# Kernel optimization log

Hardware: AMD Instinct MI355X
Metric: run time of the kernel (lower is better)

The kernel has to match this reference:

```python
import jax, jax.numpy as jnp
import numpy as np

EPS = 1e-5

def _ln(x, g, b):
    mu = jnp.mean(x, axis=-1, keepdims=True)
    var = jnp.mean(jnp.square(x - mu), axis=-1, keepdims=True)
    return (x - mu) * jax.lax.rsqrt(var + EPS) * g + b

def setup_inputs() -> dict:
    key = jax.random.key(0)
    ks = jax.random.split(key, 16)
    B, L, D, H = 1, 512, 128, 128  # d_pair=128, d_hidden=128
    s_d = 1.0 / np.sqrt(D)
    s_h = 1.0 / np.sqrt(H)
    return {
        "pair": jax.random.normal(ks[0], (B, L, L, D), jnp.float32),
        "ln_g": jnp.ones((D,), jnp.float32),
        "ln_b": jnp.zeros((D,), jnp.float32),
        "lw": jax.random.normal(ks[1], (H, D), jnp.float32) * s_d,
        "lb": jnp.zeros((H,), jnp.float32),
        "lgw": jax.random.normal(ks[2], (H, D), jnp.float32) * s_d,
        "lgb": jnp.ones((H,), jnp.float32),
        "rw": jax.random.normal(ks[3], (H, D), jnp.float32) * s_d,
        "rb": jnp.zeros((H,), jnp.float32),
        "rgw": jax.random.normal(ks[4], (H, D), jnp.float32) * s_d,
        "rgb": jnp.ones((H,), jnp.float32),
        "gw": jax.random.normal(ks[5], (D, D), jnp.float32) * s_d,
        "gb": jnp.ones((D,), jnp.float32),
        "lno_g": jnp.ones((H,), jnp.float32),
        "lno_b": jnp.zeros((H,), jnp.float32),
        "ow": jax.random.normal(ks[6], (D, H), jnp.float32) * s_h,
        "ob": jnp.zeros((D,), jnp.float32),
    }

def reference(pair, ln_g, ln_b, lw, lb, lgw, lgb, rw, rb, rgw, rgb, gw, gb, lno_g, lno_b, ow, ob):
    L = pair.shape[1]
    p = _ln(pair, ln_g, ln_b)                                   # [B,L,L,D]
    left = jax.nn.sigmoid(p @ lgw.T + lgb) * (p @ lw.T + lb)    # [B,L,L,H]
    right = jax.nn.sigmoid(p @ rgw.T + rgb) * (p @ rw.T + rb)   # [B,L,L,H]
    # outgoing: contract over k (second seq dim)
    out = jnp.einsum('bikd,bjkd->bijd', left, right / jnp.float32(L))
    out = _ln(out, lno_g, lno_b)
    out = out @ ow.T + ob                                       # [B,L,L,D]
    gate = jax.nn.sigmoid(p @ gw.T + gb)
    return gate * out
```

## Files before the change

### kernel.cpp

```cpp
#include <hip/hip_runtime.h>
#include <hip/hip_bf16.h>
#include <stdint.h>

#define LSEQ 512
#define LL   262144

typedef __attribute__((ext_vector_type(8))) short short8;
typedef __attribute__((ext_vector_type(4))) float f32x4;
typedef __attribute__((ext_vector_type(4))) unsigned short us4;
typedef __attribute__((ext_vector_type(8))) unsigned short us8;

static_assert(sizeof(short8) == 16, "");
static_assert(sizeof(us8) == 16, "");

__device__ inline unsigned short f2bf(float f){
  unsigned u = __builtin_bit_cast(unsigned, f);
  unsigned r = (u + 0x7fffu + ((u >> 16) & 1u)) >> 16;
  return (unsigned short)r;
}
__device__ inline float bf2f(unsigned short s){
  return __builtin_bit_cast(float, ((unsigned)s) << 16);
}
__device__ inline float sigm(float x){ return 1.f / (1.f + __expf(-x)); }

__device__ inline int sw256(int row, int byte_in_row){
  return row*256 + ((((byte_in_row >> 4) ^ (row & 7))) << 4) + (byte_in_row & 15);
}
__device__ inline int sw128(int row, int byte_in_row){
  return row*128 + ((((byte_in_row >> 4) ^ (row & 7))) << 4) + (byte_in_row & 15);
}

__device__ inline void gload16(const void* g, void* lds){
  __builtin_amdgcn_global_load_lds(
      (const __attribute__((address_space(1))) unsigned*)g,
      (__attribute__((address_space(3))) unsigned*)lds, 16, 0, 0);
}

__global__ __launch_bounds__(128) void k0_prep(
    const float* __restrict__ ow, const float* __restrict__ lnog,
    const float* __restrict__ lnob, const float* __restrict__ ob,
    unsigned short* __restrict__ wgbf, float* __restrict__ swg, float* __restrict__ swb)
{
  const int dd = blockIdx.x;
  const int t  = threadIdx.x;
  const int idx = dd*128 + t;
  float o = ow[idx];
  float a = o * lnog[t];
  float b = o * lnob[t];
  wgbf[idx] = f2bf(a);
  #pragma unroll
  for (int m = 1; m < 64; m <<= 1){ a += __shfl_xor(a, m); b += __shfl_xor(b, m); }
  __shared__ float sA[2], sB[2];
  if ((t & 63) == 0){ sA[t >> 6] = a; sB[t >> 6] = b; }
  __syncthreads();
  if (t == 0){ swg[dd] = sA[0] + sA[1]; swb[dd] = sB[0] + sB[1] + ob[dd]; }
}

__global__ __launch_bounds__(64) void kP_pack(
    const float* __restrict__ lgw, const float* __restrict__ lw,
    const float* __restrict__ rgw, const float* __restrict__ rw,
    const float* __restrict__ gw, short8* __restrict__ wpk)
{
  const int b = blockIdx.x;
  const int arm = b >> 5, n = (b >> 2) & 7, ks = b & 3;
  const float* src = arm==0 ? lgw : arm==1 ? lw : arm==2 ? rgw : arm==3 ? rw : gw;
  const int l = threadIdx.x;
  const int h = n*16 + (l & 15), k0 = ks*32 + (l >> 4)*8;
  short8 v;
  #pragma unroll
  for (int e = 0; e < 8; ++e) v[e] = (short)f2bf(src[h*128 + k0 + e]);
  wpk[b*64 + l] = v;
}

__global__ __launch_bounds__(256, 4) void k1_proj(
    const float* __restrict__ pair, const float* __restrict__ ln_g, const float* __restrict__ ln_b,
    const float* __restrict__ lb,  const float* __restrict__ lgb,
    const float* __restrict__ rb,  const float* __restrict__ rgb,
    const float* __restrict__ gb,
    const short8* __restrict__ wpk,
    unsigned short* __restrict__ lt, unsigned short* __restrict__ rt,
    unsigned short* __restrict__ gate)
{
  __shared__ char p_l[16384];
  const int t = threadIdx.x;
  const int w = t >> 6, l = t & 63;
  const long pos0 = (long)blockIdx.x * 64;

  {
    const int q8 = t & 7;
    float4 g4[4], b4[4];
    #pragma unroll
    for (int i = 0; i < 4; ++i){
      g4[i] = *(const float4*)(ln_g + q8*4 + i*32);
      b4[i] = *(const float4*)(ln_b + q8*4 + i*32);
    }
    #pragma unroll
    for (int pass = 0; pass < 2; ++pass){
      const int row = pass*32 + (t >> 3);
      float4 x[4];
      #pragma unroll
      for (int i = 0; i < 4; ++i)
        x[i] = *(const float4*)(pair + (pos0 + row)*128 + q8*4 + i*32);
      float s = 0.f, qq = 0.f;
      #pragma unroll
      for (int i = 0; i < 4; ++i){
        s  += (x[i].x + x[i].y) + (x[i].z + x[i].w);
        qq += (x[i].x*x[i].x + x[i].y*x[i].y) + (x[i].z*x[i].z + x[i].w*x[i].w);
      }
      #pragma unroll
      for (int msk = 1; msk < 8; msk <<= 1){ s += __shfl_xor(s, msk); qq += __shfl_xor(qq, msk); }
      const float mu = s * (1.f/128.f);
      const float rs = rsqrtf(qq * (1.f/128.f) - mu*mu + 1e-5f);
      #pragma unroll
      for (int i = 0; i < 4; ++i){
        us4 o;
        o.x = f2bf((x[i].x - mu)*rs*g4[i].x + b4[i].x);
        o.y = f2bf((x[i].y - mu)*rs*g4[i].y + b4[i].y);
        o.z = f2bf((x[i].z - mu)*rs*g4[i].z + b4[i].z);
        o.w = f2bf((x[i].w - mu)*rs*g4[i].w + b4[i].w);
        *(us4*)(p_l + sw256(row, q8*8 + i*64)) = o;
      }
    }
  }
  __syncthreads();

  f32x4 aG[4][2], aL[4][2];
  auto zero = [&](f32x4 (&acc)[4][2]){
    #pragma unroll
    for (int m = 0; m < 4; ++m){ acc[m][0] = f32x4{0,0,0,0}; acc[m][1] = f32x4{0,0,0,0}; }
  };
  auto gemm2 = [&](int armG, int armL){
    #pragma unroll
    for (int ks = 0; ks < 4; ++ks){
      short8 av[4];
      #pragma unroll
      for (int m = 0; m < 4; ++m)
        av[m] = *(const short8*)(p_l + sw256(m*16 + (l & 15), ks*64 + (l >> 4)*16));
      #pragma unroll
      for (int n2 = 0; n2 < 2; ++n2){
        const int n = w*2 + n2;
        const short8 bg = wpk[((armG*8 + n)*4 + ks)*64 + l];
        const short8 bl = wpk[((armL*8 + n)*4 + ks)*64 + l];
        #pragma unroll
        for (int m = 0; m < 4; ++m){
          aG[m][n2] = __builtin_amdgcn_mfma_f32_16x16x32_bf16(av[m], bg, aG[m][n2], 0, 0, 0);
          aL[m][n2] = __builtin_amdgcn_mfma_f32_16x16x32_bf16(av[m], bl, aL[m][n2], 0, 0, 0);
        }
      }
    }
  };
  auto epiDirect = [&](const float* __restrict__ gbias, const float* __restrict__ lbias,
                       unsigned short* __restrict__ dst){
    #pragma unroll
    for (int n2 = 0; n2 < 2; ++n2){
      const int h = w*32 + n2*16 + (l & 15);
      const float gv = gbias[h], lv = lbias[h];
      #pragma unroll
      for (int m = 0; m < 4; ++m){
        us4 o;
        #pragma unroll
        for (int r = 0; r < 4; ++r)
          o[r] = f2bf(sigm(aG[m][n2][r] + gv) * (aL[m][n2][r] + lv));
        *(us4*)(dst + (long)h*LL + pos0 + m*16 + (l >> 4)*4) = o;
      }
    }
  };

  zero(aG); zero(aL); gemm2(0, 1); epiDirect(lgb, lb, lt);
  zero(aG); zero(aL); gemm2(2, 3); epiDirect(rgb, rb, rt);

  zero(aG);
  #pragma unroll
  for (int ks = 0; ks < 4; ++ks){
    short8 av[4];
    #pragma unroll
    for (int m = 0; m < 4; ++m)
      av[m] = *(const short8*)(p_l + sw256(m*16 + (l & 15), ks*64 + (l >> 4)*16));
    #pragma unroll
    for (int n2 = 0; n2 < 2; ++n2){
      const int n = w*2 + n2;
      const short8 bg = wpk[((4*8 + n)*4 + ks)*64 + l];
      #pragma unroll
      for (int m = 0; m < 4; ++m)
        aG[m][n2] = __builtin_amdgcn_mfma_f32_16x16x32_bf16(av[m], bg, aG[m][n2], 0, 0, 0);
    }
  }
  __syncthreads();
  #pragma unroll
  for (int n2 = 0; n2 < 2; ++n2){
    const int h = w*32 + n2*16 + (l & 15);
    const float gv = gb[h];
    #pragma unroll
    for (int m = 0; m < 4; ++m)
      #pragma unroll
      for (int r = 0; r < 4; ++r){
        const int pos = m*16 + (l >> 4)*4 + r;
        *(unsigned short*)(p_l + sw256(pos, h*2)) = f2bf(sigm(aG[m][n2][r] + gv));
      }
  }
  __syncthreads();
  #pragma unroll
  for (int p = 0; p < 4; ++p){
    const int row = p*16 + (t >> 4), ch = t & 15;
    us8 v = *(const us8*)(p_l + sw256(row, ch*16));
    *(us8*)(gate + (pos0 + row)*128 + ch*8) = v;
  }
}

__global__ __launch_bounds__(256) void k2_tri(
    const unsigned short* __restrict__ lt, const unsigned short* __restrict__ rt,
    unsigned short* __restrict__ omm)
{
  __shared__ char smem[32768];
  char* As = smem;
  char* Bs = smem + 16384;
  const int t = threadIdx.x;
  const int b0 = blockIdx.x;
  const int b  = (b0 & 7) * 256 + (b0 >> 3);
  const int d = b >> 4, tile = b & 15;
  const int i0 = (tile >> 2)*128, j0 = (tile & 3)*128;
  const unsigned short* Ag = lt + (long)d*LL;
  const unsigned short* Bg = rt + (long)d*LL;
  const int w = t >> 6, l = t & 63;
  const int wm = w >> 1, wn = w & 1;

  f32x4 acc[4][4];
  #pragma unroll
  for (int m = 0; m < 4; ++m)
    #pragma unroll
    for (int n = 0; n < 4; ++n) acc[m][n] = f32x4{0.f,0.f,0.f,0.f};

  for (int kt = 0; kt < 8; ++kt){
    const int k0 = kt*64;
    __syncthreads();
    #pragma unroll
    for (int q = 0; q < 4; ++q){
      int P = q*4096 + t*16;
      int row = P >> 7;
      int ls  = ((P >> 4) & 7) ^ (row & 7);
      gload16(Ag + (long)(i0 + row)*512 + k0 + ls*8, As + P);
      gload16(Bg + (long)(j0 + row)*512 + k0 + ls*8, Bs + P);
    }
    __syncthreads();
    #pragma unroll
    for (int ks = 0; ks < 2; ++ks){
      short8 a[4], bb[4];
      #pragma unroll
      for (int m = 0; m < 4; ++m){
        int row = wm*64 + m*16 + (l & 15);
        a[m] = *(const short8*)(As + sw128(row, ks*64 + (l >> 4)*16));
      }
      #pragma unroll
      for (int n = 0; n < 4; ++n){
        int row = wn*64 + n*16 + (l & 15);
        bb[n] = *(const short8*)(Bs + sw128(row, ks*64 + (l >> 4)*16));
      }
      #pragma unroll
      for (int m = 0; m < 4; ++m)
        #pragma unroll
        for (int n = 0; n < 4; ++n)
          acc[m][n] = __builtin_amdgcn_mfma_f32_16x16x32_bf16(a[m], bb[n], acc[m][n], 0, 0, 0);
    }
  }
  __syncthreads();
  #pragma unroll
  for (int m = 0; m < 4; ++m)
    #pragma unroll
    for (int n = 0; n < 4; ++n)
      #pragma unroll
      for (int r = 0; r < 4; ++r){
        int row = wm*64 + m*16 + (l >> 4)*4 + r;
        int j   = wn*64 + n*16 + (l & 15);
        *(unsigned short*)(smem + sw256(row, j*2)) = f2bf(acc[m][n][r] * (1.f/512.f));
      }
  __syncthreads();
  #pragma unroll
  for (int it = 0; it < 8; ++it){
    int row = it*16 + (t >> 4), ch = t & 15;
    us8 v = *(const us8*)(smem + sw256(row, ch*16));
    *(us8*)(omm + (long)d*LL + (long)(i0 + row)*512 + j0 + ch*8) = v;
  }
}

__global__ __launch_bounds__(256) void k3_out(
    const unsigned short* __restrict__ omm, const unsigned short* __restrict__ gate,
    const unsigned short* __restrict__ wgbf,
    const float* __restrict__ swg, const float* __restrict__ swb,
    float* __restrict__ out)
{
  __shared__ char omm_l[32768];
  __shared__ char wg_l[32768];
  __shared__ float mu_s[128], rs_s[128];
  const int t = threadIdx.x;
  const int jt = blockIdx.x, i = blockIdx.y;
  const int j0 = jt*128;
  const int w = t >> 6, l = t & 63;

  {
    const int jc = t & 15, dg = t >> 4;
    float sum[8], sq[8];
    #pragma unroll
    for (int e = 0; e < 8; ++e){ sum[e] = 0.f; sq[e] = 0.f; }
    #pragma unroll
    for (int q = 0; q < 8; ++q){
      int dd = dg + q*16;
      us8 v = *(const us8*)(omm + (long)dd*LL + (long)i*512 + j0 + jc*8);
      *(us8*)(omm_l + dd*256 + jc*16) = v;
      #pragma unroll
      for (int e = 0; e < 8; ++e){
        float f = bf2f(v[e]);
        sum[e] += f; sq[e] += f*f;
      }
    }
    float* scr = (float*)wg_l;
    #pragma unroll
    for (int e = 0; e < 8; ++e){
      scr[dg*128 + jc*8 + e]        = sum[e];
      scr[2048 + dg*128 + jc*8 + e] = sq[e];
    }
  }
  __syncthreads();
  if (t < 128){
    const float* scr = (const float*)wg_l;
    float s1 = 0.f, s2 = 0.f;
    #pragma unroll
    for (int g = 0; g < 16; ++g){ s1 += scr[g*128 + t]; s2 += scr[2048 + g*128 + t]; }
    float mu = s1 * (1.f/128.f);
    float var = s2 * (1.f/128.f) - mu*mu;
    mu_s[t] = mu;
    rs_s[t] = rsqrtf(var + 1e-5f);
  }
  __syncthreads();
  #pragma unroll
  for (int q = 0; q < 8; ++q){
    int P = q*4096 + t*16;
    gload16((const char*)wgbf + sw256(P >> 8, P & 255), wg_l + P);
  }
  __syncthreads();

  f32x4 acc[2][8];
  #pragma unroll
  for (int m = 0; m < 2; ++m)
    #pragma unroll
    for (int n = 0; n < 8; ++n) acc[m][n] = f32x4{0.f,0.f,0.f,0.f};

  #pragma unroll
  for (int ks = 0; ks < 4; ++ks){
    short8 a[2];
    #pragma unroll
    for (int m = 0; m < 2; ++m){
      const int jj = w*32 + m*16 + (l & 15);
      short8 av;
      #pragma unroll
      for (int e = 0; e < 8; ++e){
        int dd = ks*32 + (l >> 4)*8 + e;
        av[e] = *(const short*)(omm_l + dd*256 + jj*2);
      }
      a[m] = av;
    }
    #pragma unroll
    for (int n = 0; n < 8; ++n){
      int row = n*16 + (l & 15);
      short8 bb = *(const short8*)(wg_l + sw256(row, ks*64 + (l >> 4)*16));
      #pragma unroll
      for (int m = 0; m < 2; ++m)
        acc[m][n] = __builtin_amdgcn_mfma_f32_16x16x32_bf16(a[m], bb, acc[m][n], 0, 0, 0);
    }
  }

  float swgv[8], swbv[8];
  #pragma unroll
  for (int n = 0; n < 8; ++n){ swgv[n] = swg[n*16 + (l & 15)]; swbv[n] = swb[n*16 + (l & 15)]; }
  #pragma unroll
  for (int m = 0; m < 2; ++m){
    #pragma unroll
    for (int r = 0; r < 4; ++r){
      int j = w*32 + m*16 + (l >> 4)*4 + r;
      float mu = mu_s[j], rs = rs_s[j];
      long rowoff = ((long)i*512 + j0 + j)*128;
      #pragma unroll
      for (int n = 0; n < 8; ++n){
        int ddx = n*16 + (l & 15);
        float val = rs*(acc[m][n][r] - mu*swgv[n]) + swbv[n];
        out[rowoff + ddx] = val * bf2f(gate[rowoff + ddx]);
      }
    }
  }
}

extern "C" void kernel_launch(void* const* d_in, const int* in_sizes, int n_in,
                              void* d_out, int out_size, void* d_ws, size_t ws_size,
                              hipStream_t stream)
{
  const float* pair = (const float*)d_in[0];
  const float* ln_g = (const float*)d_in[1];
  const float* ln_b = (const float*)d_in[2];
  const float* lw   = (const float*)d_in[3];
  const float* lb   = (const float*)d_in[4];
  const float* lgw  = (const float*)d_in[5];
  const float* lgb  = (const float*)d_in[6];
  const float* rw   = (const float*)d_in[7];
  const float* rb   = (const float*)d_in[8];
  const float* rgw  = (const float*)d_in[9];
  const float* rgb  = (const float*)d_in[10];
  const float* gw   = (const float*)d_in[11];
  const float* gb   = (const float*)d_in[12];
  const float* lnog = (const float*)d_in[13];
  const float* lnob = (const float*)d_in[14];
  const float* ow   = (const float*)d_in[15];
  const float* ob   = (const float*)d_in[16];
  float* out = (float*)d_out;

  char* ws = (char*)d_ws;
  unsigned short* lt   = (unsigned short*)(ws);
  unsigned short* rt   = (unsigned short*)(ws + (1l << 26));
  unsigned short* gate = (unsigned short*)(ws + (2l << 26));
  unsigned short* omm  = (unsigned short*)(ws + (3l << 26));
  short8*         wpk  = (short8*)(ws + (3l << 26));
  unsigned short* wgbf = (unsigned short*)(ws + (4l << 26));
  float* swg = (float*)(ws + (4l << 26) + 65536);
  float* swb = swg + 128;

  k0_prep<<<dim3(128), dim3(128), 0, stream>>>(ow, lnog, lnob, ob, wgbf, swg, swb);
  kP_pack<<<dim3(160), dim3(64), 0, stream>>>(lgw, lw, rgw, rw, gw, wpk);
  k1_proj<<<dim3(4096), dim3(256), 0, stream>>>(pair, ln_g, ln_b, lb, lgb, rb, rgb, gb,
                                                wpk, lt, rt, gate);
  k2_tri<<<dim3(2048), dim3(256), 0, stream>>>(lt, rt, omm);
  k3_out<<<dim3(4, 512), dim3(256), 0, stream>>>(omm, gate, wgbf, swg, swb, out);
}
```

Before: 338.3 us.

## Switch to fp16 MFMA, stage gate in output buffer, fold weight prep into kernels

Converts all intermediate storage and MFMA ops from bf16 to fp16. The gate is written as fp32 straight into the output buffer and read back in the final kernel, which removes the separate gate workspace. The projection epilogue transposes through an LDS buffer so global stores are coalesced. The separate prep kernel is removed: each k3 block recomputes the folded LN weights itself. The triangle kernel now loads tiles through registers instead of direct global-to-LDS loads. Each k3 block repeats the 128x128 weight folding, and the fp32 gate adds write and read traffic.

```diff
diff --git a/kernel.cpp b/kernel.cpp
--- a/kernel.cpp
+++ b/kernel.cpp
@@ -5,21 +5,20 @@
 #define LSEQ 512
 #define LL   262144
 
-typedef __attribute__((ext_vector_type(8))) short short8;
+typedef __attribute__((ext_vector_type(8))) _Float16 half8;
 typedef __attribute__((ext_vector_type(4))) float f32x4;
 typedef __attribute__((ext_vector_type(4))) unsigned short us4;
 typedef __attribute__((ext_vector_type(8))) unsigned short us8;
 
-static_assert(sizeof(short8) == 16, "");
+static_assert(sizeof(half8) == 16, "");
 static_assert(sizeof(us8) == 16, "");
 
-__device__ inline unsigned short f2bf(float f){
-  unsigned u = __builtin_bit_cast(unsigned, f);
-  unsigned r = (u + 0x7fffu + ((u >> 16) & 1u)) >> 16;
-  return (unsigned short)r;
-}
-__device__ inline float bf2f(unsigned short s){
-  return __builtin_bit_cast(float, ((unsigned)s) << 16);
+__device__ inline unsigned short f2h(float f){
+  _Float16 h = (_Float16)f;
+  return __builtin_bit_cast(unsigned short, h);
+}
+__device__ inline float h2f(unsigned short s){
+  return (float)__builtin_bit_cast(_Float16, s);
 }
 __device__ inline float sigm(float x){ return 1.f / (1.f + __expf(-x)); }
 
@@ -28,47 +27,21 @@
 }
 __device__ inline int sw128(int row, int byte_in_row){
   return row*128 + ((((byte_in_row >> 4) ^ (row & 7))) << 4) + (byte_in_row & 15);
-}
-
-__device__ inline void gload16(const void* g, void* lds){
-  __builtin_amdgcn_global_load_lds(
-      (const __attribute__((address_space(1))) unsigned*)g,
-      (__attribute__((address_space(3))) unsigned*)lds, 16, 0, 0);
-}
-
-__global__ __launch_bounds__(128) void k0_prep(
-    const float* __restrict__ ow, const float* __restrict__ lnog,
-    const float* __restrict__ lnob, const float* __restrict__ ob,
-    unsigned short* __restrict__ wgbf, float* __restrict__ swg, float* __restrict__ swb)
-{
-  const int dd = blockIdx.x;
-  const int t  = threadIdx.x;
-  const int idx = dd*128 + t;
-  float o = ow[idx];
-  float a = o * lnog[t];
-  float b = o * lnob[t];
-  wgbf[idx] = f2bf(a);
-  #pragma unroll
-  for (int m = 1; m < 64; m <<= 1){ a += __shfl_xor(a, m); b += __shfl_xor(b, m); }
-  __shared__ float sA[2], sB[2];
-  if ((t & 63) == 0){ sA[t >> 6] = a; sB[t >> 6] = b; }
-  __syncthreads();
-  if (t == 0){ swg[dd] = sA[0] + sA[1]; swb[dd] = sB[0] + sB[1] + ob[dd]; }
 }
 
 __global__ __launch_bounds__(64) void kP_pack(
     const float* __restrict__ lgw, const float* __restrict__ lw,
     const float* __restrict__ rgw, const float* __restrict__ rw,
-    const float* __restrict__ gw, short8* __restrict__ wpk)
+    const float* __restrict__ gw, us8* __restrict__ wpk)
 {
   const int b = blockIdx.x;
   const int arm = b >> 5, n = (b >> 2) & 7, ks = b & 3;
   const float* src = arm==0 ? lgw : arm==1 ? lw : arm==2 ? rgw : arm==3 ? rw : gw;
   const int l = threadIdx.x;
   const int h = n*16 + (l & 15), k0 = ks*32 + (l >> 4)*8;
-  short8 v;
-  #pragma unroll
-  for (int e = 0; e < 8; ++e) v[e] = (short)f2bf(src[h*128 + k0 + e]);
+  us8 v;
+  #pragma unroll
+  for (int e = 0; e < 8; ++e) v[e] = f2h(src[h*128 + k0 + e]);
   wpk[b*64 + l] = v;
 }
 
@@ -77,11 +50,12 @@
     const float* __restrict__ lb,  const float* __restrict__ lgb,
     const float* __restrict__ rb,  const float* __restrict__ rgb,
     const float* __restrict__ gb,
-    const short8* __restrict__ wpk,
+    const us8* __restrict__ wpk,
     unsigned short* __restrict__ lt, unsigned short* __restrict__ rt,
-    unsigned short* __restrict__ gate)
+    float* __restrict__ outg)
 {
   __shared__ char p_l[16384];
+  __shared__ char epi[16384];
   const int t = threadIdx.x;
   const int w = t >> 6, l = t & 63;
   const long pos0 = (long)blockIdx.x * 64;
@@ -114,10 +88,10 @@
       #pragma unroll
       for (int i = 0; i < 4; ++i){
         us4 o;
-        o.x = f2bf((x[i].x - mu)*rs*g4[i].x + b4[i].x);
-        o.y = f2bf((x[i].y - mu)*rs*g4[i].y + b4[i].y);
-        o.z = f2bf((x[i].z - mu)*rs*g4[i].z + b4[i].z);
-        o.w = f2bf((x[i].w - mu)*rs*g4[i].w + b4[i].w);
+        o.x = f2h((x[i].x - mu)*rs*g4[i].x + b4[i].x);
+        o.y = f2h((x[i].y - mu)*rs*g4[i].y + b4[i].y);
+        o.z = f2h((x[i].z - mu)*rs*g4[i].z + b4[i].z);
+        o.w = f2h((x[i].w - mu)*rs*g4[i].w + b4[i].w);
         *(us4*)(p_l + sw256(row, q8*8 + i*64)) = o;
       }
     }
@@ -132,25 +106,25 @@
   auto gemm2 = [&](int armG, int armL){
     #pragma unroll
     for (int ks = 0; ks < 4; ++ks){
-      short8 av[4];
+      half8 av[4];
       #pragma unroll
       for (int m = 0; m < 4; ++m)
-        av[m] = *(const short8*)(p_l + sw256(m*16 + (l & 15), ks*64 + (l >> 4)*16));
+        av[m] = *(const half8*)(p_l + sw256(m*16 + (l & 15), ks*64 + (l >> 4)*16));
       #pragma unroll
       for (int n2 = 0; n2 < 2; ++n2){
         const int n = w*2 + n2;
-        const short8 bg = wpk[((armG*8 + n)*4 + ks)*64 + l];
-        const short8 bl = wpk[((armL*8 + n)*4 + ks)*64 + l];
+        const half8 bg = __builtin_bit_cast(half8, wpk[(armG*32 + n*4 + ks)*64 + l]);
+        const half8 bl = __builtin_bit_cast(half8, wpk[(armL*32 + n*4 + ks)*64 + l]);
         #pragma unroll
         for (int m = 0; m < 4; ++m){
-          aG[m][n2] = __builtin_amdgcn_mfma_f32_16x16x32_bf16(av[m], bg, aG[m][n2], 0, 0, 0);
-          aL[m][n2] = __builtin_amdgcn_mfma_f32_16x16x32_bf16(av[m], bl, aL[m][n2], 0, 0, 0);
+          aG[m][n2] = __builtin_amdgcn_mfma_f32_16x16x32_f16(av[m], bg, aG[m][n2], 0, 0, 0);
+          aL[m][n2] = __builtin_amdgcn_mfma_f32_16x16x32_f16(av[m], bl, aL[m][n2], 0, 0, 0);
         }
       }
     }
   };
-  auto epiDirect = [&](const float* __restrict__ gbias, const float* __restrict__ lbias,
-                       unsigned short* __restrict__ dst){
+  auto epiT = [&](const float* __restrict__ gbias, const float* __restrict__ lbias,
+                  unsigned short* __restrict__ dst){
     #pragma unroll
     for (int n2 = 0; n2 < 2; ++n2){
       const int h = w*32 + n2*16 + (l & 15);
@@ -160,32 +134,39 @@
         us4 o;
         #pragma unroll
         for (int r = 0; r < 4; ++r)
-          o[r] = f2bf(sigm(aG[m][n2][r] + gv) * (aL[m][n2][r] + lv));
-        *(us4*)(dst + (long)h*LL + pos0 + m*16 + (l >> 4)*4) = o;
-      }
-    }
+          o[r] = f2h(sigm(aG[m][n2][r] + gv) * (aL[m][n2][r] + lv));
+        *(us4*)(epi + sw128(h, (m*16 + (l >> 4)*4)*2)) = o;
+      }
+    }
+    __syncthreads();
+    #pragma unroll
+    for (int p = 0; p < 4; ++p){
+      const int hh = p*32 + (t >> 3), ch = t & 7;
+      us8 v = *(const us8*)(epi + sw128(hh, ch*16));
+      *(us8*)(dst + (long)hh*LL + pos0 + ch*8) = v;
+    }
+    __syncthreads();
   };
 
-  zero(aG); zero(aL); gemm2(0, 1); epiDirect(lgb, lb, lt);
-  zero(aG); zero(aL); gemm2(2, 3); epiDirect(rgb, rb, rt);
+  zero(aG); zero(aL); gemm2(0, 1); epiT(lgb, lb, lt);
+  zero(aG); zero(aL); gemm2(2, 3); epiT(rgb, rb, rt);
 
   zero(aG);
   #pragma unroll
   for (int ks = 0; ks < 4; ++ks){
-    short8 av[4];
+    half8 av[4];
     #pragma unroll
     for (int m = 0; m < 4; ++m)
-      av[m] = *(const short8*)(p_l + sw256(m*16 + (l & 15), ks*64 + (l >> 4)*16));
+      av[m] = *(const half8*)(p_l + sw256(m*16 + (l & 15), ks*64 + (l >> 4)*16));
     #pragma unroll
     for (int n2 = 0; n2 < 2; ++n2){
       const int n = w*2 + n2;
-      const short8 bg = wpk[((4*8 + n)*4 + ks)*64 + l];
+      const half8 bg = __builtin_bit_cast(half8, wpk[(4*32 + n*4 + ks)*64 + l]);
       #pragma unroll
       for (int m = 0; m < 4; ++m)
-        aG[m][n2] = __builtin_amdgcn_mfma_f32_16x16x32_bf16(av[m], bg, aG[m][n2], 0, 0, 0);
-    }
-  }
-  __syncthreads();
+        aG[m][n2] = __builtin_amdgcn_mfma_f32_16x16x32_f16(av[m], bg, aG[m][n2], 0, 0, 0);
+    }
+  }
   #pragma unroll
   for (int n2 = 0; n2 < 2; ++n2){
     const int h = w*32 + n2*16 + (l & 15);
@@ -195,15 +176,8 @@
       #pragma unroll
       for (int r = 0; r < 4; ++r){
         const int pos = m*16 + (l >> 4)*4 + r;
-        *(unsigned short*)(p_l + sw256(pos, h*2)) = f2bf(sigm(aG[m][n2][r] + gv));
-      }
-  }
-  __syncthreads();
-  #pragma unroll
-  for (int p = 0; p < 4; ++p){
-    const int row = p*16 + (t >> 4), ch = t & 15;
-    us8 v = *(const us8*)(p_l + sw256(row, ch*16));
-    *(us8*)(gate + (pos0 + row)*128 + ch*8) = v;
+        outg[(pos0 + pos)*128 + h] = sigm(aG[m][n2][r] + gv);
+      }
   }
 }
 
@@ -232,34 +206,43 @@
 
   for (int kt = 0; kt < 8; ++kt){
     const int k0 = kt*64;
+    us8 ra[4], rb[4];
+    #pragma unroll
+    for (int q = 0; q < 4; ++q){
+      const int P = q*4096 + t*16;
+      const int row = P >> 7;
+      const int slot = (P >> 4) & 7;
+      ra[q] = *(const us8*)(Ag + (long)(i0 + row)*512 + k0 + slot*8);
+      rb[q] = *(const us8*)(Bg + (long)(j0 + row)*512 + k0 + slot*8);
+    }
     __syncthreads();
     #pragma unroll
     for (int q = 0; q < 4; ++q){
-      int P = q*4096 + t*16;
-      int row = P >> 7;
-      int ls  = ((P >> 4) & 7) ^ (row & 7);
-      gload16(Ag + (long)(i0 + row)*512 + k0 + ls*8, As + P);
-      gload16(Bg + (long)(j0 + row)*512 + k0 + ls*8, Bs + P);
+      const int P = q*4096 + t*16;
+      const int row = P >> 7;
+      const int ds = P ^ ((row & 7) << 4);
+      *(us8*)(As + ds) = ra[q];
+      *(us8*)(Bs + ds) = rb[q];
     }
     __syncthreads();
     #pragma unroll
     for (int ks = 0; ks < 2; ++ks){
-      short8 a[4], bb[4];
+      half8 a[4], bb[4];
       #pragma unroll
       for (int m = 0; m < 4; ++m){
         int row = wm*64 + m*16 + (l & 15);
-        a[m] = *(const short8*)(As + sw128(row, ks*64 + (l >> 4)*16));
+        a[m] = *(const half8*)(As + sw128(row, ks*64 + (l >> 4)*16));
       }
       #pragma unroll
       for (int n = 0; n < 4; ++n){
         int row = wn*64 + n*16 + (l & 15);
-        bb[n] = *(const short8*)(Bs + sw128(row, ks*64 + (l >> 4)*16));
+        bb[n] = *(const half8*)(Bs + sw128(row, ks*64 + (l >> 4)*16));
       }
       #pragma unroll
       for (int m = 0; m < 4; ++m)
         #pragma unroll
         for (int n = 0; n < 4; ++n)
-          acc[m][n] = __builtin_amdgcn_mfma_f32_16x16x32_bf16(a[m], bb[n], acc[m][n], 0, 0, 0);
+          acc[m][n] = __builtin_amdgcn_mfma_f32_16x16x32_f16(a[m], bb[n], acc[m][n], 0, 0, 0);
     }
   }
   __syncthreads();
@@ -271,7 +254,7 @@
       for (int r = 0; r < 4; ++r){
         int row = wm*64 + m*16 + (l >> 4)*4 + r;
         int j   = wn*64 + n*16 + (l & 15);
-        *(unsigned short*)(smem + sw256(row, j*2)) = f2bf(acc[m][n][r] * (1.f/512.f));
+        *(unsigned short*)(smem + sw256(row, j*2)) = f2h(acc[m][n][r] * (1.f/512.f));
       }
   __syncthreads();
   #pragma unroll
@@ -283,14 +266,14 @@
 }
 
 __global__ __launch_bounds__(256) void k3_out(
-    const unsigned short* __restrict__ omm, const unsigned short* __restrict__ gate,
-    const unsigned short* __restrict__ wgbf,
-    const float* __restrict__ swg, const float* __restrict__ swb,
-    float* __restrict__ out)
+    const unsigned short* __restrict__ omm,
+    const float* __restrict__ ow, const float* __restrict__ lnog,
+    const float* __restrict__ lnob, const float* __restrict__ ob,
+    float* out)
 {
   __shared__ char omm_l[32768];
   __shared__ char wg_l[32768];
-  __shared__ float mu_s[128], rs_s[128];
+  __shared__ float mu_s[128], rs_s[128], swg_s[128], swb_s[128];
   const int t = threadIdx.x;
   const int jt = blockIdx.x, i = blockIdx.y;
   const int j0 = jt*128;
@@ -308,7 +291,7 @@
       *(us8*)(omm_l + dd*256 + jc*16) = v;
       #pragma unroll
       for (int e = 0; e < 8; ++e){
-        float f = bf2f(v[e]);
+        float f = h2f(v[e]);
         sum[e] += f; sq[e] += f*f;
       }
     }
@@ -329,12 +312,29 @@
     float var = s2 * (1.f/128.f) - mu*mu;
     mu_s[t] = mu;
     rs_s[t] = rsqrtf(var + 1e-5f);
-  }
-  __syncthreads();
-  #pragma unroll
-  for (int q = 0; q < 8; ++q){
-    int P = q*4096 + t*16;
-    gload16((const char*)wgbf + sw256(P >> 8, P & 255), wg_l + P);
+    float sg = 0.f, sb = 0.f;
+    const float* owr = ow + t*128;
+    for (int d = 0; d < 128; ++d){
+      float o = owr[d];
+      sg += o * lnog[d];
+      sb += o * lnob[d];
+    }
+    swg_s[t] = sg;
+    swb_s[t] = sb + ob[t];
+  }
+  __syncthreads();
+  {
+    #pragma unroll
+    for (int it = 0; it < 16; ++it){
+      const int idx4 = (it*256 + t)*4;
+      const int row = idx4 >> 7, col = idx4 & 127;
+      const float4 o4 = *(const float4*)(ow + idx4);
+      const float4 g4 = *(const float4*)(lnog + col);
+      us4 v;
+      v.x = f2h(o4.x*g4.x); v.y = f2h(o4.y*g4.y);
+      v.z = f2h(o4.z*g4.z); v.w = f2h(o4.w*g4.w);
+      *(us4*)(wg_l + sw256(row, col*2)) = v;
+    }
   }
   __syncthreads();
 
@@ -346,31 +346,32 @@
 
   #pragma unroll
   for (int ks = 0; ks < 4; ++ks){
-    short8 a[2];
+    us8 a[2];
     #pragma unroll
     for (int m = 0; m < 2; ++m){
       const int jj = w*32 + m*16 + (l & 15);
-      short8 av;
+      us8 av;
       #pragma unroll
       for (int e = 0; e < 8; ++e){
         int dd = ks*32 + (l >> 4)*8 + e;
-        av[e] = *(const short*)(omm_l + dd*256 + jj*2);
+        av[e] = *(const unsigned short*)(omm_l + dd*256 + jj*2);
       }
       a[m] = av;
     }
     #pragma unroll
     for (int n = 0; n < 8; ++n){
       int row = n*16 + (l & 15);
-      short8 bb = *(const short8*)(wg_l + sw256(row, ks*64 + (l >> 4)*16));
+      half8 bb = *(const half8*)(wg_l + sw256(row, ks*64 + (l >> 4)*16));
       #pragma unroll
       for (int m = 0; m < 2; ++m)
-        acc[m][n] = __builtin_amdgcn_mfma_f32_16x16x32_bf16(a[m], bb, acc[m][n], 0, 0, 0);
+        acc[m][n] = __builtin_amdgcn_mfma_f32_16x16x32_f16(
+            __builtin_bit_cast(half8, a[m]), bb, acc[m][n], 0, 0, 0);
     }
   }
 
   float swgv[8], swbv[8];
   #pragma unroll
-  for (int n = 0; n < 8; ++n){ swgv[n] = swg[n*16 + (l & 15)]; swbv[n] = swb[n*16 + (l & 15)]; }
+  for (int n = 0; n < 8; ++n){ swgv[n] = swg_s[n*16 + (l & 15)]; swbv[n] = swb_s[n*16 + (l & 15)]; }
   #pragma unroll
   for (int m = 0; m < 2; ++m){
     #pragma unroll
@@ -381,8 +382,9 @@
       #pragma unroll
       for (int n = 0; n < 8; ++n){
         int ddx = n*16 + (l & 15);
+        float gv = out[rowoff + ddx];
         float val = rs*(acc[m][n][r] - mu*swgv[n]) + swbv[n];
-        out[rowoff + ddx] = val * bf2f(gate[rowoff + ddx]);
+        out[rowoff + ddx] = val * gv;
       }
     }
   }
@@ -414,17 +416,12 @@
   char* ws = (char*)d_ws;
   unsigned short* lt   = (unsigned short*)(ws);
   unsigned short* rt   = (unsigned short*)(ws + (1l << 26));
-  unsigned short* gate = (unsigned short*)(ws + (2l << 26));
+  us8*            wpk  = (us8*)(ws + (2l << 26));
   unsigned short* omm  = (unsigned short*)(ws + (3l << 26));
-  short8*         wpk  = (short8*)(ws + (3l << 26));
-  unsigned short* wgbf = (unsigned short*)(ws + (4l << 26));
-  float* swg = (float*)(ws + (4l << 26) + 65536);
-  float* swb = swg + 128;
-
-  k0_prep<<<dim3(128), dim3(128), 0, stream>>>(ow, lnog, lnob, ob, wgbf, swg, swb);
+
   kP_pack<<<dim3(160), dim3(64), 0, stream>>>(lgw, lw, rgw, rw, gw, wpk);
   k1_proj<<<dim3(4096), dim3(256), 0, stream>>>(pair, ln_g, ln_b, lb, lgb, rb, rgb, gb,
-                                                wpk, lt, rt, gate);
+                                                wpk, lt, rt, out);
   k2_tri<<<dim3(2048), dim3(256), 0, stream>>>(lt, rt, omm);
-  k3_out<<<dim3(4, 512), dim3(256), 0, stream>>>(omm, gate, wgbf, swg, swb, out);
-}
+  k3_out<<<dim3(4, 512), dim3(256), 0, stream>>>(omm, ow, lnog, lnob, ob, out);
+}
```

After: 320.9 us. -5.2%, faster.
